# Optimization experiments

Hardware: AMD Instinct MI355X
Metric: run time of the kernel (lower is better)

The kernel has to match this reference:

```python
import jax, jax.numpy as jnp
import numpy as np

IN_DIM = 64; OUT_DIM = 128; B = 4; N = 256
GRID_SIZE = 5; ORDER = 3; NUM_BASIS = GRID_SIZE + ORDER  # 8
EPS_LN = 1e-5; EPS_BN = 1e-5; TEMP = 1.0

def make_grid():
    g = jnp.linspace(-1.0, 1.0, GRID_SIZE + 1)
    h = 2.0 / GRID_SIZE
    left = g[0] - h * jnp.arange(ORDER, 0, -1, dtype=jnp.float32)
    right = g[-1] + h * jnp.arange(1, ORDER + 1, dtype=jnp.float32)
    return jnp.concatenate([left, g, right])  # (grid_size+1+2*order,) = (12,)

def kan_layer(x, base_w, spline_w, coeffs):
    # x: (rows, in_features); eval mode (dropout = identity)
    grid = make_grid()
    x = jnp.tanh(x)
    base_out = jax.nn.silu(x) @ base_w.T
    xe = x[..., None]  # (rows, in, 1)
    bases = ((xe >= grid[:-1]) & (xe < grid[1:])).astype(x.dtype)  # (rows, in, 11)
    for k in range(1, ORDER + 1):  # Cox-de Boor recursion
        dl = jnp.clip(grid[k:-1] - grid[:-k - 1], 1e-8)
        dr = jnp.clip(grid[k + 1:] - grid[1:-k], 1e-8)
        bases = (xe - grid[:-k - 1]) / dl * bases[..., :-1] + (grid[k + 1:] - xe) / dr * bases[..., 1:]
    # bases: (rows, in, NUM_BASIS)
    sc = jnp.clip(coeffs, -5.0, 5.0) * spline_w[..., None]  # (out, in, NUM_BASIS)
    return base_out + jnp.einsum('bij,oij->bo', bases, sc)

def layer_norm(x, g, b):
    m = x.mean(-1, keepdims=True)
    v = x.var(-1, keepdims=True)
    return (x - m) * jax.lax.rsqrt(v + EPS_LN) * g + b

def setup_inputs() -> dict:
    key = jax.random.key(0)
    ks = jax.random.split(key, 12)
    def r(k, shape, s=1.0):
        return jax.random.normal(k, shape, jnp.float32) * s
    return {
        "h": r(ks[0], (B, N, IN_DIM)),
        "ln_in_g": jnp.ones((IN_DIM,), jnp.float32), "ln_in_b": jnp.zeros((IN_DIM,), jnp.float32),
        "ln_p_g": jnp.ones((IN_DIM,), jnp.float32), "ln_p_b": jnp.zeros((IN_DIM,), jnp.float32),
        "ka_bw": r(ks[1], (IN_DIM, IN_DIM), 0.05), "ka_sw": r(ks[2], (IN_DIM, IN_DIM), 0.05),
        "ka_c": r(ks[3], (IN_DIM, IN_DIM, NUM_BASIS), 0.001),
        "W_att": r(ks[4], (IN_DIM, N), 0.05),
        "kp_bw": r(ks[5], (OUT_DIM, IN_DIM), 0.05), "kp_sw": r(ks[6], (OUT_DIM, IN_DIM), 0.05),
        "kp_c": r(ks[7], (OUT_DIM, IN_DIM, NUM_BASIS), 0.001),
        "kd_bw": r(ks[8], (OUT_DIM, IN_DIM), 0.05), "kd_sw": r(ks[9], (OUT_DIM, IN_DIM), 0.05),
        "kd_c": r(ks[10], (OUT_DIM, IN_DIM, NUM_BASIS), 0.001),
        "bn_g": jnp.ones((OUT_DIM,), jnp.float32), "bn_b": jnp.zeros((OUT_DIM,), jnp.float32),
        "bn_mean": r(ks[11], (OUT_DIM,), 0.1), "bn_var": jnp.ones((OUT_DIM,), jnp.float32),
    }

def reference(h, ln_in_g, ln_in_b, ln_p_g, ln_p_b, ka_bw, ka_sw, ka_c, W_att,
              kp_bw, kp_sw, kp_c, kd_bw, kd_sw, kd_c, bn_g, bn_b, bn_mean, bn_var):
    b, n, d = h.shape
    h = layer_norm(h, ln_in_g, ln_in_b)
    hn = h / jnp.clip(jnp.linalg.norm(h, axis=-1, keepdims=True), 1e-12)
    prod = hn[:, :, None, :] * hn[:, None, :, :]          # (B, N, N, D) pairwise products
    prod = layer_norm(prod, ln_p_g, ln_p_b)
    kan_out = jnp.tanh(kan_layer(prod.reshape(-1, d), ka_bw, ka_sw, ka_c)).reshape(b, n, n, d)
    # einsum('bnmd,dk->bnmk') followed by mean over k == contraction with mean of W_att over k
    w_mean = W_att.mean(axis=1)                           # (D,)
    scores = jnp.einsum('bnmd,d->bnm', kan_out, w_mean)
    attn = jax.nn.softmax(scores / (jnp.sqrt(jnp.float32(d)) * TEMP), axis=-1)
    h_att = jnp.einsum('bnm,bmd->bnd', attn, h)
    out2 = kan_layer(h_att.reshape(-1, d), kp_bw, kp_sw, kp_c).reshape(b, n, OUT_DIM)
    out3 = kan_layer(h.reshape(-1, d), kd_bw, kd_sw, kd_c).reshape(b, n, OUT_DIM)
    out = out2 + out3
    # BatchNorm1d over channel dim, eval mode (running stats)
    out = (out - bn_mean) * jax.lax.rsqrt(bn_var + EPS_BN) * bn_g + bn_b
    return out
```

## Files before the change

kernel.cpp:

```cpp
#include <hip/hip_runtime.h>
#include <hip/hip_bf16.h>
#include <stdint.h>

#define BBATCH 4
#define NSEQ   256
#define DIN    64
#define DOUT   128
#define NBASIS 8
#define KTOT   576
#define K2TOT  1152
#define NSTEP  18
#define XST16  68
#define NJOBS  1152

typedef __attribute__((ext_vector_type(8))) __bf16 bf16x8;
typedef __attribute__((ext_vector_type(4))) float  f32x4;

__device__ __forceinline__ float wave_sum(float v){
#pragma unroll
  for (int m = 1; m < 64; m <<= 1) v += __shfl_xor(v, m, 64);
  return v;
}

__device__ __forceinline__ float fast_tanh(float y){
  y = fminf(10.f, fmaxf(-10.f, y));
  float e = __expf(2.f * y);
  return (e - 1.f) / (e + 1.f);
}

__device__ __forceinline__ float silu_f(float x){
  return __fdividef(x, 1.f + __expf(-x));
}

__device__ __forceinline__ unsigned short f2bf(float f){
  union { float f; unsigned u; } v; v.f = f;
  unsigned r = (v.u + 0x7fffu + ((v.u >> 16) & 1u)) >> 16;
  return (unsigned short)r;
}

__device__ __forceinline__ float bf2f(unsigned short s){
  union { unsigned u; float f; } v; v.u = ((unsigned)s) << 16;
  return v.f;
}

__device__ __forceinline__ float bf2f_lo(unsigned w){
  union { unsigned u; float f; } v; v.u = w << 16;
  return v.f;
}
__device__ __forceinline__ float bf2f_hi(unsigned w){
  union { unsigned u; float f; } v; v.u = w & 0xffff0000u;
  return v.f;
}

__device__ __forceinline__ unsigned pk2(float a, float b){
  union { float f; unsigned u; } ua, ub; ua.f = a; ub.f = b;
  return __builtin_amdgcn_perm(ub.u + 0x8000u, ua.u + 0x8000u, 0x07060302);
}

__device__ __forceinline__ void spline_w(float x, int &i, float w[4]){
  float u = (x + 1.f) * 2.5f;
  int ii = (int)floorf(u);
  ii = ii < 0 ? 0 : (ii > 5 ? 5 : ii);
  float t = u - (float)ii;
  float t2 = t * t, t3 = t2 * t;
  float it = 1.f - t;
  w[0] = it * it * it * (1.f/6.f);
  w[1] = (3.f*t3 - 6.f*t2 + 4.f) * (1.f/6.f);
  w[2] = (-3.f*t3 + 3.f*t2 + 3.f*t + 1.f) * (1.f/6.f);
  w[3] = t3 * (1.f/6.f);
  i = ii;
}

__device__ __forceinline__ bf16x8 spline_pack(float x){
  float u = (x + 1.f) * 2.5f;
  int ii = (int)floorf(u);
  ii = ii < 0 ? 0 : (ii > 5 ? 5 : ii);
  float t = u - (float)ii;
  float t2 = t * t, t3 = t2 * t;
  float it = 1.f - t;
  float w0 = it * it * it * (1.f/6.f);
  float w1 = (3.f*t3 - 6.f*t2 + 4.f) * (1.f/6.f);
  float w2 = (-3.f*t3 + 3.f*t2 + 3.f*t + 1.f) * (1.f/6.f);
  float w3 = t3 * (1.f/6.f);
  unsigned long long W = ((unsigned long long)pk2(w2, w3) << 32) | (unsigned long long)pk2(w0, w1);
  int s16 = ii << 4;
  unsigned long long shl_lo = W << (s16 & 63);
  unsigned long long shr    = W >> ((64 - s16) & 63);
  unsigned long long shl_hi = W << ((s16 - 64) & 63);
  bool ge4 = ii >= 4;
  unsigned long long lo = ge4 ? 0ull : shl_lo;
  unsigned long long hi = ge4 ? shl_hi : (ii == 0 ? 0ull : shr);
  union { unsigned long long q[2]; bf16x8 v8; } r;
  r.q[0] = lo; r.q[1] = hi;
  return r.v8;
}

__global__ void k_prep_all(const float* __restrict__ h,
                           const float* __restrict__ g_in, const float* __restrict__ b_in,
                           const float* __restrict__ ka_bw, const float* __restrict__ ka_sw,
                           const float* __restrict__ ka_c,  const float* __restrict__ W_att,
                           const float* __restrict__ kp_bw, const float* __restrict__ kp_sw,
                           const float* __restrict__ kp_c,
                           const float* __restrict__ kd_bw, const float* __restrict__ kd_sw,
                           const float* __restrict__ kd_c,
                           float* __restrict__ h_ln, float* __restrict__ hn,
                           unsigned short* __restrict__ S_t, float* __restrict__ wm,
                           unsigned short* __restrict__ S2,
                           unsigned short* __restrict__ jobs){
  int blk = blockIdx.x, tid = threadIdx.x;
  if (blk < 256){
    int row = blk*4 + (tid >> 6);
    int d   = tid & 63;
    float x = h[row*DIN + d];
    float mean = wave_sum(x) * (1.f/64.f);
    float xm = x - mean;
    float var = wave_sum(xm*xm) * (1.f/64.f);
    float hl = xm * rsqrtf(var + 1e-5f) * g_in[d] + b_in[d];
    h_ln[row*DIN + d] = hl;
    float nrm = sqrtf(wave_sum(hl*hl));
    nrm = fmaxf(nrm, 1e-12f);
    hn[row*DIN + d] = hl / nrm;
  } else if (blk < 320){
    int o = blk - 256;
    int nt = o >> 4, colr = o & 15;
    for (int k = tid; k < KTOT; k += 256){
      float v;
      if (k < 64){
        v = ka_bw[o*64 + k];
      } else {
        int km = k - 64, dd = km >> 3, j = km & 7;
        float c = ka_c[(o*64 + dd)*8 + j];
        c = fminf(5.f, fmaxf(-5.f, c));
        v = c * ka_sw[o*64 + dd];
      }
      int s = k >> 5, grp = (k >> 3) & 3, e = k & 7;
      int lane = grp*16 + colr;
      S_t[((s*4 + nt)*64 + lane)*8 + e] = f2bf(v);
    }
  } else if (blk == 320){
    if (tid < 64){
      float s = 0.f;
      for (int k = 0; k < 256; ++k) s += W_att[tid*256 + k];
      wm[tid] = s * (1.f/256.f);
    }
    const int offs[9] = {0,256,480,672,832,960,1056,1120,1152};
    for (int f = tid; f < NJOBS; f += 256){
      int t = 0;
      while (f >= offs[t+1]) ++t;
      int r = f - offs[t];
      int n = t*32 + r / (8 - t);
      int w = t + r % (8 - t);
      jobs[f] = (unsigned short)((n << 3) | w);
    }
  } else {
    int o = blk - 321;
    for (int kk = tid; kk < K2TOT; kk += 256){
      const float* bw; const float* sw; const float* cc;
      int k = kk;
      if (kk < KTOT){ bw = kp_bw; sw = kp_sw; cc = kp_c; }
      else          { bw = kd_bw; sw = kd_sw; cc = kd_c; k = kk - KTOT; }
      float v;
      if (k < 64){
        v = bw[o*64 + k];
      } else {
        int km = k - 64, d = km >> 3, j = km & 7;
        float c = cc[(o*64 + d)*8 + j];
        c = fminf(5.f, fmaxf(-5.f, c));
        v = c * sw[o*64 + d];
      }
      S2[((kk >> 3)*128 + o)*8 + (kk & 7)] = f2bf(v);
    }
  }
}

__launch_bounds__(512, 4)
__global__ void k_scores(const float* __restrict__ hn,
                         const float* __restrict__ ln_p_g, const float* __restrict__ ln_p_b,
                         const unsigned short* __restrict__ S_t,
                         const float* __restrict__ wm,
                         const unsigned short* __restrict__ jobs,
                         float* __restrict__ scores){
  __shared__ unsigned short Xs[NSEQ * XST16];
  __shared__ float hnn_l[8][64];
  __shared__ float g_l[64], b_l[64];

  int blkid = blockIdx.x;
  int bb    = blkid / 144;
  int jb    = (blkid % 144) * 8;

  int tid  = threadIdx.x;
  int lane = tid & 63, wave = tid >> 6;
  int job  = jobs[jb + wave];
  int n    = job >> 3;
  int w    = job & 7;
  int sn   = n >> 5;
  int m0g  = w * 32;
  int lr0  = wave * 32;

  g_l[lane] = ln_p_g[lane];
  b_l[lane] = ln_p_b[lane];
  hnn_l[wave][lane] = bf2f(f2bf(hn[(bb*NSEQ + n)*DIN + lane]));

  {
    const float* src = hn + (bb*NSEQ + m0g)*DIN;
#pragma unroll
    for (int j = 0; j < 8; ++j){
      int f4 = j*64 + lane;
      float4 v = *(const float4*)(src + f4*4);
      int r = f4 >> 4, c = (f4 & 15) * 4;
      uint2 pk = { pk2(v.x, v.y), pk2(v.z, v.w) };
      *(uint2*)(Xs + (lr0 + r)*XST16 + c) = pk;
    }
  }

  {
    int r = lane >> 1, hh = lane & 1;
    unsigned short* row = Xs + (lr0 + r)*XST16 + hh*32;
    const float* hp = hnn_l[wave] + hh*32;
    float s1 = 0.f, s2 = 0.f;
#pragma unroll
    for (int i = 0; i < 8; ++i){
      uint2 ww = *(const uint2*)(row + i*4);
      float x0 = bf2f_lo(ww.x), x1 = bf2f_hi(ww.x), x2 = bf2f_lo(ww.y), x3 = bf2f_hi(ww.y);
      float p0 = x0*hp[i*4+0], p1 = x1*hp[i*4+1], p2 = x2*hp[i*4+2], p3 = x3*hp[i*4+3];
      s1 += (p0+p1) + (p2+p3);
      s2 = fmaf(p0,p0, fmaf(p1,p1, fmaf(p2,p2, fmaf(p3,p3, s2))));
    }
    s1 += __shfl_xor(s1, 1, 64);
    s2 += __shfl_xor(s2, 1, 64);
    float mean = s1 * (1.f/64.f);
    float var  = fmaxf(s2 * (1.f/64.f) - mean*mean, 0.f);
    float inv  = rsqrtf(var + 1e-5f);
    const float* gp = g_l + hh*32;
    const float* bp = b_l + hh*32;
#pragma unroll
    for (int i = 0; i < 8; ++i){
      uint2 ww = *(const uint2*)(row + i*4);
      float x0 = bf2f_lo(ww.x), x1 = bf2f_hi(ww.x), x2 = bf2f_lo(ww.y), x3 = bf2f_hi(ww.y);
      float t0 = fast_tanh((x0*hp[i*4+0] - mean)*inv*gp[i*4+0] + bp[i*4+0]);
      float t1 = fast_tanh((x1*hp[i*4+1] - mean)*inv*gp[i*4+1] + bp[i*4+1]);
      float t2 = fast_tanh((x2*hp[i*4+2] - mean)*inv*gp[i*4+2] + bp[i*4+2]);
      float t3 = fast_tanh((x3*hp[i*4+3] - mean)*inv*gp[i*4+3] + bp[i*4+3]);
      uint2 pk = { pk2(t0, t1), pk2(t2, t3) };
      *(uint2*)(row + i*4) = pk;
    }
  }

  int colr = lane & 15, grp = lane >> 4;
  const unsigned short* rowA = Xs + (lr0 + colr)*XST16;
  const unsigned short* rowB = Xs + (lr0 + 16 + colr)*XST16;
  const unsigned short* sfp  = S_t + lane*8;

  f32x4 acc[2][4];
#pragma unroll
  for (int a = 0; a < 2; ++a)
#pragma unroll
    for (int c = 0; c < 4; ++c){ f32x4 z = {0.f,0.f,0.f,0.f}; acc[a][c] = z; }

#pragma unroll
  for (int s = 0; s < 2; ++s){
    int kw = s*32 + grp*8;
    bf16x8 bf[4];
#pragma unroll
    for (int nt = 0; nt < 4; ++nt)
      bf[nt] = *(const bf16x8*)(sfp + (s*4 + nt)*512);
    union { unsigned u[4]; bf16x8 v8; } a0, a1;
    uint2 wa0 = *(const uint2*)(rowA + kw), wa1 = *(const uint2*)(rowA + kw + 4);
    uint2 wb0 = *(const uint2*)(rowB + kw), wb1 = *(const uint2*)(rowB + kw + 4);
    a0.u[0] = pk2(silu_f(bf2f_lo(wa0.x)), silu_f(bf2f_hi(wa0.x)));
    a0.u[1] = pk2(silu_f(bf2f_lo(wa0.y)), silu_f(bf2f_hi(wa0.y)));
    a0.u[2] = pk2(silu_f(bf2f_lo(wa1.x)), silu_f(bf2f_hi(wa1.x)));
    a0.u[3] = pk2(silu_f(bf2f_lo(wa1.y)), silu_f(bf2f_hi(wa1.y)));
    a1.u[0] = pk2(silu_f(bf2f_lo(wb0.x)), silu_f(bf2f_hi(wb0.x)));
    a1.u[1] = pk2(silu_f(bf2f_lo(wb0.y)), silu_f(bf2f_hi(wb0.y)));
    a1.u[2] = pk2(silu_f(bf2f_lo(wb1.x)), silu_f(bf2f_hi(wb1.x)));
    a1.u[3] = pk2(silu_f(bf2f_lo(wb1.y)), silu_f(bf2f_hi(wb1.y)));
#pragma unroll
    for (int nt = 0; nt < 4; ++nt){
      acc[0][nt] = __builtin_amdgcn_mfma_f32_16x16x32_bf16(a0.v8, bf[nt], acc[0][nt], 0, 0, 0);
      acc[1][nt] = __builtin_amdgcn_mfma_f32_16x16x32_bf16(a1.v8, bf[nt], acc[1][nt], 0, 0, 0);
    }
  }

#pragma unroll 4
  for (int s = 2; s < NSTEP; ++s){
    int d  = (s - 2)*4 + grp;
    bf16x8 bf[4];
#pragma unroll
    for (int nt = 0; nt < 4; ++nt)
      bf[nt] = *(const bf16x8*)(sfp + (s*4 + nt)*512);
    bf16x8 a0 = spline_pack(bf2f(rowA[d]));
    bf16x8 a1 = spline_pack(bf2f(rowB[d]));
#pragma unroll
    for (int nt = 0; nt < 4; ++nt){
      acc[0][nt] = __builtin_amdgcn_mfma_f32_16x16x32_bf16(a0, bf[nt], acc[0][nt], 0, 0, 0);
      acc[1][nt] = __builtin_amdgcn_mfma_f32_16x16x32_bf16(a1, bf[nt], acc[1][nt], 0, 0, 0);
    }
  }

  float wmv[4];
#pragma unroll
  for (int nt = 0; nt < 4; ++nt) wmv[nt] = wm[nt*16 + colr];

#pragma unroll
  for (int a = 0; a < 2; ++a){
    float sacc[4] = {0.f,0.f,0.f,0.f};
#pragma unroll
    for (int nt = 0; nt < 4; ++nt){
#pragma unroll
      for (int r = 0; r < 4; ++r)
        sacc[r] += fast_tanh(acc[a][nt][r]) * wmv[nt];
    }
#pragma unroll
    for (int off = 1; off < 16; off <<= 1){
#pragma unroll
      for (int r = 0; r < 4; ++r) sacc[r] += __shfl_xor(sacc[r], off, 64);
    }
    if (colr == 0){
      int mb   = m0g + a*16 + grp*4;
      int base = (bb*NSEQ + n)*NSEQ + mb;
      float4 v = { sacc[0], sacc[1], sacc[2], sacc[3] };
      *(float4*)&scores[base] = v;
      if (w > sn){
        int tb = bb*NSEQ*NSEQ + n;
#pragma unroll
        for (int r = 0; r < 4; ++r)
          scores[tb + (mb + r)*NSEQ] = sacc[r];
      }
    }
  }
}

__launch_bounds__(256, 4)
__global__ void k_smf(const float* __restrict__ scores,
                      const float* __restrict__ h_ln,
                      const unsigned short* __restrict__ S2,
                      const float* __restrict__ bn_g, const float* __restrict__ bn_b,
                      const float* __restrict__ bn_mean, const float* __restrict__ bn_var,
                      float* __restrict__ out){
  __shared__ float att[2][256];
  __shared__ float redm[2][2], reds[2][2];
  __shared__ float part[2][2][64];
  __shared__ float hatt[2][64];
  __shared__ float feat[2][K2TOT];
  int row0 = blockIdx.x * 2;
  int tid = threadIdx.x, lane = tid & 63, wave = tid >> 6;
  int rw = wave >> 1;
  int qw = wave & 1;
  int row = row0 + rw;
  int t128 = (qw << 6) | lane;

  float s0 = scores[row*NSEQ + t128] * 0.125f;
  float s1 = scores[row*NSEQ + 128 + t128] * 0.125f;
  float mx = fmaxf(s0, s1);
#pragma unroll
  for (int off = 1; off < 64; off <<= 1) mx = fmaxf(mx, __shfl_xor(mx, off, 64));
  if (lane == 0) redm[rw][qw] = mx;
  __syncthreads();
  mx = fmaxf(redm[rw][0], redm[rw][1]);
  float e0 = __expf(s0 - mx), e1 = __expf(s1 - mx);
  float es = wave_sum(e0 + e1);
  if (lane == 0) reds[rw][qw] = es;
  __syncthreads();
  float tot = reds[rw][0] + reds[rw][1];
  att[rw][t128]       = e0 / tot;
  att[rw][128 + t128] = e1 / tot;
  __syncthreads();

  int hb = row & ~255;
  float a2 = 0.f;
  for (int m = qw*128; m < qw*128 + 128; ++m)
    a2 += att[rw][m] * h_ln[(hb + m)*DIN + lane];
  part[rw][qw][lane] = a2;
  __syncthreads();
  if (qw == 0)
    hatt[rw][lane] = part[rw][0][lane] + part[rw][1][lane];
  __syncthreads();

  {
    int src = t128 >> 6, dd = t128 & 63;
    float x = src ? h_ln[row*DIN + dd] : hatt[rw][dd];
    x = fast_tanh(x);
    int base = src * KTOT;
    feat[rw][base + dd] = silu_f(x);
    int fb = base + 64 + dd*8;
#pragma unroll
    for (int jj = 0; jj < 8; ++jj) feat[rw][fb + jj] = 0.f;
    int i; float wgt[4];
    spline_w(x, i, wgt);
#pragma unroll
    for (int k = 0; k < 4; ++k){
      int jj = i + k;
      if (jj < 8) feat[rw][fb + jj] = wgt[k];
    }
  }
  __syncthreads();

  int o = t128;
  const unsigned short* sp = S2 + o*8;
  const float* fp = feat[rw];
  float acc = 0.f;
#pragma unroll 4
  for (int jj = 0; jj < K2TOT/8; ++jj){
    uint4  w  = *(const uint4*)(sp + jj*1024);
    float4 f0 = *(const float4*)(fp + jj*8);
    float4 f1 = *(const float4*)(fp + jj*8 + 4);
    acc = fmaf(f0.x, bf2f_lo(w.x), acc);
    acc = fmaf(f0.y, bf2f_hi(w.x), acc);
    acc = fmaf(f0.z, bf2f_lo(w.y), acc);
    acc = fmaf(f0.w, bf2f_hi(w.y), acc);
    acc = fmaf(f1.x, bf2f_lo(w.z), acc);
    acc = fmaf(f1.y, bf2f_hi(w.z), acc);
    acc = fmaf(f1.z, bf2f_lo(w.w), acc);
    acc = fmaf(f1.w, bf2f_hi(w.w), acc);
  }
  float r = (acc - bn_mean[o]) * rsqrtf(bn_var[o] + 1e-5f) * bn_g[o] + bn_b[o];
  out[row*DOUT + o] = r;
}

extern "C" void kernel_launch(void* const* d_in, const int* in_sizes, int n_in,
                              void* d_out, int out_size, void* d_ws, size_t ws_size,
                              hipStream_t stream){
  (void)in_sizes; (void)n_in; (void)out_size; (void)ws_size;
  const float* h       = (const float*)d_in[0];
  const float* ln_in_g = (const float*)d_in[1];
  const float* ln_in_b = (const float*)d_in[2];
  const float* ln_p_g  = (const float*)d_in[3];
  const float* ln_p_b  = (const float*)d_in[4];
  const float* ka_bw   = (const float*)d_in[5];
  const float* ka_sw   = (const float*)d_in[6];
  const float* ka_c    = (const float*)d_in[7];
  const float* W_att   = (const float*)d_in[8];
  const float* kp_bw   = (const float*)d_in[9];
  const float* kp_sw   = (const float*)d_in[10];
  const float* kp_c    = (const float*)d_in[11];
  const float* kd_bw   = (const float*)d_in[12];
  const float* kd_sw   = (const float*)d_in[13];
  const float* kd_c    = (const float*)d_in[14];
  const float* bn_g    = (const float*)d_in[15];
  const float* bn_b    = (const float*)d_in[16];
  const float* bn_mean = (const float*)d_in[17];
  const float* bn_var  = (const float*)d_in[18];
  float* out = (float*)d_out;

  char* ws = (char*)d_ws;
  float*          h_ln   = (float*)(ws + 0);
  float*          hn     = (float*)(ws + 262144);
  unsigned short* S_t    = (unsigned short*)(ws + 524288);
  float*          wm     = (float*)(ws + 598016);
  float*          scores = (float*)(ws + 598272);
  unsigned short* jobs   = (unsigned short*)(ws + 1646848);
  unsigned short* S2     = (unsigned short*)(ws + 1908992);

  k_prep_all<<<449, 256, 0, stream>>>(h, ln_in_g, ln_in_b, ka_bw, ka_sw, ka_c, W_att,
                                      kp_bw, kp_sw, kp_c, kd_bw, kd_sw, kd_c,
                                      h_ln, hn, S_t, wm, S2, jobs);
  k_scores<<<576, 512, 0, stream>>>(hn, ln_p_g, ln_p_b, S_t, wm, jobs, scores);
  k_smf<<<512, 256, 0, stream>>>(scores, h_ln, S2, bn_g, bn_b, bn_mean, bn_var, out);
}
```

Before: 76.63 us.

## Halve k_scores block size and split k_smf KAN reduction across twice the threads

k_scores now runs 4 waves per block over 128 key rows instead of 8 waves over 256, doubling the block count and halving shared memory per block. k_smf doubles threads per block: softmax uses one element per thread, the attention-weighted sum is split four ways, and the final KAN dot product over the 1152 features is split into two halves combined through shared memory. The aim is more parallelism and shorter serial loops per thread. The cost is an extra barrier and reduction step, and the k_scores change relies on the hidden staging loops still matching the smaller tile.

```diff
diff --git a/kernel.cpp b/kernel.cpp
--- a/kernel.cpp
+++ b/kernel.cpp
@@ -173,20 +173,20 @@
   }
 }
 
-__launch_bounds__(512, 4)
+__launch_bounds__(256, 4)
 __global__ void k_scores(const float* __restrict__ hn,
                          const float* __restrict__ ln_p_g, const float* __restrict__ ln_p_b,
                          const unsigned short* __restrict__ S_t,
                          const float* __restrict__ wm,
                          const unsigned short* __restrict__ jobs,
                          float* __restrict__ scores){
-  __shared__ unsigned short Xs[NSEQ * XST16];
-  __shared__ float hnn_l[8][64];
+  __shared__ unsigned short Xs[128 * XST16];
+  __shared__ float hnn_l[4][64];
   __shared__ float g_l[64], b_l[64];
 
   int blkid = blockIdx.x;
-  int bb    = blkid / 144;
-  int jb    = (blkid % 144) * 8;
+  int bb    = blkid / 288;
+  int jb    = (blkid % 288) * 4;
 
   int tid  = threadIdx.x;
   int lane = tid & 63, wave = tid >> 6;
@@ -331,7 +331,7 @@
   }
 }
 
-__launch_bounds__(256, 4)
+__launch_bounds__(512, 4)
 __global__ void k_smf(const float* __restrict__ scores,
                       const float* __restrict__ h_ln,
                       const unsigned short* __restrict__ S2,
@@ -339,46 +339,46 @@
                       const float* __restrict__ bn_mean, const float* __restrict__ bn_var,
                       float* __restrict__ out){
   __shared__ float att[2][256];
-  __shared__ float redm[2][2], reds[2][2];
-  __shared__ float part[2][2][64];
+  __shared__ float redm[2][4], reds[2][4];
+  __shared__ float part[2][4][64];
   __shared__ float hatt[2][64];
   __shared__ float feat[2][K2TOT];
+  __shared__ float pout[2][128];
   int row0 = blockIdx.x * 2;
-  int tid = threadIdx.x, lane = tid & 63, wave = tid >> 6;
-  int rw = wave >> 1;
-  int qw = wave & 1;
-  int row = row0 + rw;
-  int t128 = (qw << 6) | lane;
-
-  float s0 = scores[row*NSEQ + t128] * 0.125f;
-  float s1 = scores[row*NSEQ + 128 + t128] * 0.125f;
-  float mx = fmaxf(s0, s1);
+  int tid = threadIdx.x, lane = tid & 63;
+  int rw   = tid >> 8;
+  int wv4  = (tid >> 6) & 3;
+  int t256 = tid & 255;
+  int row  = row0 + rw;
+
+  float sc = scores[row*NSEQ + t256] * 0.125f;
+  float mx = sc;
 #pragma unroll
   for (int off = 1; off < 64; off <<= 1) mx = fmaxf(mx, __shfl_xor(mx, off, 64));
-  if (lane == 0) redm[rw][qw] = mx;
-  __syncthreads();
-  mx = fmaxf(redm[rw][0], redm[rw][1]);
-  float e0 = __expf(s0 - mx), e1 = __expf(s1 - mx);
-  float es = wave_sum(e0 + e1);
-  if (lane == 0) reds[rw][qw] = es;
-  __syncthreads();
-  float tot = reds[rw][0] + reds[rw][1];
-  att[rw][t128]       = e0 / tot;
-  att[rw][128 + t128] = e1 / tot;
+  if (lane == 0) redm[rw][wv4] = mx;
+  __syncthreads();
+  mx = fmaxf(fmaxf(redm[rw][0], redm[rw][1]), fmaxf(redm[rw][2], redm[rw][3]));
+  float e = __expf(sc - mx);
+  float es = wave_sum(e);
+  if (lane == 0) reds[rw][wv4] = es;
+  __syncthreads();
+  float tot = (reds[rw][0] + reds[rw][1]) + (reds[rw][2] + reds[rw][3]);
+  att[rw][t256] = e / tot;
   __syncthreads();
 
   int hb = row & ~255;
   float a2 = 0.f;
-  for (int m = qw*128; m < qw*128 + 128; ++m)
+  for (int m = wv4*64; m < wv4*64 + 64; ++m)
     a2 += att[rw][m] * h_ln[(hb + m)*DIN + lane];
-  part[rw][qw][lane] = a2;
-  __syncthreads();
-  if (qw == 0)
-    hatt[rw][lane] = part[rw][0][lane] + part[rw][1][lane];
-  __syncthreads();
-
-  {
-    int src = t128 >> 6, dd = t128 & 63;
+  part[rw][wv4][lane] = a2;
+  __syncthreads();
+  if (wv4 == 0)
+    hatt[rw][lane] = (part[rw][0][lane] + part[rw][1][lane])
+                   + (part[rw][2][lane] + part[rw][3][lane]);
+  __syncthreads();
+
+  if (t256 < 128){
+    int src = t256 >> 6, dd = t256 & 63;
     float x = src ? h_ln[row*DIN + dd] : hatt[rw][dd];
     x = fast_tanh(x);
     int base = src * KTOT;
@@ -396,12 +396,12 @@
   }
   __syncthreads();
 
-  int o = t128;
-  const unsigned short* sp = S2 + o*8;
-  const float* fp = feat[rw];
+  int o = t256 & 127, half = t256 >> 7;
+  const unsigned short* sp = S2 + o*8 + half*72*1024;
+  const float* fp = feat[rw] + half*576;
   float acc = 0.f;
 #pragma unroll 4
-  for (int jj = 0; jj < K2TOT/8; ++jj){
+  for (int jj = 0; jj < 72; ++jj){
     uint4  w  = *(const uint4*)(sp + jj*1024);
     float4 f0 = *(const float4*)(fp + jj*8);
     float4 f1 = *(const float4*)(fp + jj*8 + 4);
@@ -414,8 +414,13 @@
     acc = fmaf(f1.z, bf2f_lo(w.w), acc);
     acc = fmaf(f1.w, bf2f_hi(w.w), acc);
   }
-  float r = (acc - bn_mean[o]) * rsqrtf(bn_var[o] + 1e-5f) * bn_g[o] + bn_b[o];
-  out[row*DOUT + o] = r;
+  if (half) pout[rw][o] = acc;
+  __syncthreads();
+  if (!half){
+    float a = acc + pout[rw][o];
+    float r = (a - bn_mean[o]) * rsqrtf(bn_var[o] + 1e-5f) * bn_g[o] + bn_b[o];
+    out[row*DOUT + o] = r;
+  }
 }
 
 extern "C" void kernel_launch(void* const* d_in, const int* in_sizes, int n_in,
@@ -455,6 +460,6 @@
   k_prep_all<<<449, 256, 0, stream>>>(h, ln_in_g, ln_in_b, ka_bw, ka_sw, ka_c, W_att,
                                       kp_bw, kp_sw, kp_c, kd_bw, kd_sw, kd_c,
                                       h_ln, hn, S_t, wm, S2, jobs);
-  k_scores<<<576, 512, 0, stream>>>(hn, ln_p_g, ln_p_b, S_t, wm, jobs, scores);
-  k_smf<<<512, 256, 0, stream>>>(scores, h_ln, S2, bn_g, bn_b, bn_mean, bn_var, out);
-}
+  k_scores<<<1152, 256, 0, stream>>>(hn, ln_p_g, ln_p_b, S_t, wm, jobs, scores);
+  k_smf<<<512, 512, 0, stream>>>(scores, h_ln, S2, bn_g, bn_b, bn_mean, bn_var, out);
+}
```

Measured after the change: 64.46 us. 15.9% less time.
